# Kernel optimization log

Measured on AMD Instinct MI355X. Metric: run time of the kernel, lower is better.

The kernel has to match this reference:

```python
import jax, jax.numpy as jnp
import numpy as np
from jax import lax

L = 50      # observation_len
P = 30      # pred_len
N = 2048    # num nearby obstacles
EMB = 64    # embed_size
NH = 128    # node_hidden_size
EH = 256    # edge_hidden_size
AD = 64     # attention_dim
CNN = 2048  # resnet50 fc.in_features


def setup_inputs() -> dict:
    key = jax.random.key(0)
    ks = jax.random.split(key, 20)
    def rn(k, shape, s=1.0):
        return jax.random.normal(k, shape, jnp.float32) * s
    w = 0.05
    return {
        "img_embedding": rn(ks[0], (1, CNN)),
        "target_obs_pos": rn(ks[1], (1, L, 2)),
        "target_obs_pos_rel": rn(ks[2], (1, L, 2)),
        "nearby_obs_pos": rn(ks[3], (1, N, L, 2)),
        "nearby_obs_pos_rel": rn(ks[4], (1, N, L, 2)),
        "nearby_obs_hist_sizes": jax.random.randint(ks[5], (1, N, 1), 0, L + 1),
        "target_obs_hist_size": L,
        "target_h0": rn(ks[6], (NH,), w),
        "target_c0": rn(ks[7], (NH,), w),
        "W_temb": rn(ks[8], (2, EMB), w), "b_temb": jnp.zeros((EMB,), jnp.float32),
        "Wih_t": rn(ks[9], (EMB, 4 * NH), w), "Whh_t": rn(ks[10], (NH, 4 * NH), w),
        "bih_t": jnp.zeros((4 * NH,), jnp.float32), "bhh_t": jnp.zeros((4 * NH,), jnp.float32),
        "W_tatt": rn(ks[11], (2, AD), w), "b_tatt": jnp.zeros((AD,), jnp.float32),
        "nearby_h0": rn(ks[12], (EH,), w),
        "nearby_c0": rn(ks[13], (EH,), w),
        "W_nemb": rn(ks[14], (2, EMB), w), "b_nemb": jnp.zeros((EMB,), jnp.float32),
        "Wih_n": rn(ks[15], (EMB, 4 * EH), w), "Whh_n": rn(ks[16], (EH, 4 * EH), w),
        "bih_n": jnp.zeros((4 * EH,), jnp.float32), "bhh_n": jnp.zeros((4 * EH,), jnp.float32),
        "W_natt": rn(ks[17], (2, AD), w), "b_natt": jnp.zeros((AD,), jnp.float32),
        "W_pred": rn(ks[18], (NH + CNN + EH, 2), w), "b_pred": jnp.zeros((2,), jnp.float32),
    }


def _lstm_cell(x, h, c, Wih, Whh, bih, bhh, H):
    # PyTorch LSTM gate order: i, f, g, o
    g = x @ Wih + h @ Whh + bih + bhh
    i = jax.nn.sigmoid(g[..., :H])
    f = jax.nn.sigmoid(g[..., H:2 * H])
    gg = jnp.tanh(g[..., 2 * H:3 * H])
    o = jax.nn.sigmoid(g[..., 3 * H:])
    c2 = f * c + i * gg
    return o * jnp.tanh(c2), c2


def _forward(img_embedding, target_obs_pos, target_obs_pos_rel, nearby_obs_pos,
             nearby_obs_pos_rel, target_h0, target_c0, W_temb, b_temb,
             Wih_t, Whh_t, bih_t, bhh_t, W_tatt, b_tatt,
             nearby_h0, nearby_c0, W_nemb, b_nemb,
             Wih_n, Whh_n, bih_n, bhh_n, W_natt, b_natt,
             W_pred, b_pred, nearby_obs_hist_sizes, target_obs_hist_size):
    nhist = nearby_obs_hist_sizes.reshape(N)
    inv_sqrt_d = 1.0 / jnp.sqrt(jnp.float32(AD))

    def attention(trel, tpos, npos, nh, nmask, Ht_prev):
        # scores scaled by curr_N / sqrt(attention_dim), softmax over masked nearby.
        # max-subtracted softmax is mathematically identical to the original exp/sum.
        currN = jnp.sum(nmask.astype(jnp.float32))
        an = (tpos - npos) @ W_natt + b_natt          # [N, AD]
        at = trel @ W_tatt + b_tatt                   # [AD]
        scores = (an @ at) * currN * inv_sqrt_d       # [N]
        w = jax.nn.softmax(jnp.where(nmask, scores, -1e30))
        return jnp.where(currN >= 1.0, w @ nh, Ht_prev)

    def obs_step(carry, x):
        th, tc, nh, nc, Ht = carry
        t, tpos, trel, npos, nrel = x
        tmask = target_obs_hist_size > (L - t)
        nmask = nhist > (L - t)
        th2, tc2 = _lstm_cell(trel @ W_temb + b_temb, th, tc, Wih_t, Whh_t, bih_t, bhh_t, NH)
        th = jnp.where(tmask, th2, th)
        tc = jnp.where(tmask, tc2, tc)
        nh2, nc2 = _lstm_cell(nrel @ W_nemb + b_nemb, nh, nc, Wih_n, Whh_n, bih_n, bhh_n, EH)
        m = nmask[:, None]
        nh = jnp.where(m, nh2, nh)
        nc = jnp.where(m, nc2, nc)
        Ht = attention(trel, tpos, npos, nh, nmask, Ht)
        return (th, tc, nh, nc, Ht), None

    np_tm = jnp.swapaxes(nearby_obs_pos[0], 0, 1)      # [L, N, 2] time-major
    nr_tm = jnp.swapaxes(nearby_obs_pos_rel[0], 0, 1)
    xs = (jnp.arange(1, L), target_obs_pos[0, 1:], target_obs_pos_rel[0, 1:],
          np_tm[1:], nr_tm[1:])
    init = (target_h0, target_c0,
            jnp.broadcast_to(nearby_h0, (N, EH)),
            jnp.broadcast_to(nearby_c0, (N, EH)),
            nearby_h0)
    (th, tc, nh, nc, Ht), _ = lax.scan(obs_step, init, xs)

    # During prediction the original reuses nearby pos/rel from the last obs step.
    npos_last = nearby_obs_pos[0, :, L - 1, :]
    nrel_last = nearby_obs_pos_rel[0, :, L - 1, :]
    xn_last = nrel_last @ W_nemb + b_nemb
    all_mask = jnp.ones((N,), bool)

    def pred_step(carry, _):
        th, tc, nh, nc, Ht, pos = carry
        pred = jnp.concatenate([th, img_embedding[0], Ht]) @ W_pred + b_pred  # [2]
        pos = pos + pred
        th, tc = _lstm_cell(pred @ W_temb + b_temb, th, tc, Wih_t, Whh_t, bih_t, bhh_t, NH)
        nh, nc = _lstm_cell(xn_last, nh, nc, Wih_n, Whh_n, bih_n, bhh_n, EH)
        Ht = attention(pred, pos, npos_last, nh, all_mask, Ht)
        return (th, tc, nh, nc, Ht, pos), pred

    carry0 = (th, tc, nh, nc, Ht, target_obs_pos[0, L - 1])
    _, preds = lax.scan(pred_step, carry0, None, length=P)
    return preds[None]                                 # [1, P, 2]


def reference(img_embedding, target_obs_pos, target_obs_pos_rel, nearby_obs_pos,
              nearby_obs_pos_rel, nearby_obs_hist_sizes, target_obs_hist_size,
              target_h0, target_c0, W_temb, b_temb, Wih_t, Whh_t, bih_t, bhh_t,
              W_tatt, b_tatt, nearby_h0, nearby_c0, W_nemb, b_nemb,
              Wih_n, Whh_n, bih_n, bhh_n, W_natt, b_natt, W_pred, b_pred):
    return _forward(img_embedding, target_obs_pos, target_obs_pos_rel, nearby_obs_pos,
                    nearby_obs_pos_rel, target_h0, target_c0, W_temb, b_temb,
                    Wih_t, Whh_t, bih_t, bhh_t, W_tatt, b_tatt,
                    nearby_h0, nearby_c0, W_nemb, b_nemb,
                    Wih_n, Whh_n, bih_n, bhh_n, W_natt, b_natt,
                    W_pred, b_pred, nearby_obs_hist_sizes, target_obs_hist_size)
```

## Files before the change

kernel.cpp:

```cpp
#include <hip/hip_runtime.h>
#include <hip/hip_bf16.h>
#include <cstdint>

#define LH   50
#define PP   30
#define NAG  2048
#define NHID 128
#define EHID 256
#define ADIM 64
#define CNND 2048

typedef __attribute__((ext_vector_type(8))) short bf16x8;
typedef __attribute__((ext_vector_type(4))) float f32x4;

enum : int {
  WS_WT  = 0,
  WS_WZ  = 65536,
  WS_WHT = 131072,
  WS_WFN = 163840,
  WS_BFN = 165888,
  WS_WFT = 166912,
  WS_BFT = 167936,
  WS_TH  = 168448,
  WS_TC  = 168576,
  WS_W49 = 168704,
  WS_CN  = 170752,
  WS_Z   = 170756,
  WS_END = 293636
};

#define HLROW 280

__device__ __forceinline__ float sigf(float x){ return 1.0f/(1.0f + __expf(-x)); }
__device__ __forceinline__ float tanhfast(float x){
  x = fminf(15.0f, fmaxf(-15.0f, x));
  float e = __expf(2.0f*x);
  return (e - 1.0f)/(e + 1.0f);
}
__device__ __forceinline__ float bfs(short s){
  return __uint_as_float(((unsigned)(unsigned short)s) << 16);
}
__device__ __forceinline__ void gld16(const void* g, void* l){
  __builtin_amdgcn_global_load_lds(
      (const __attribute__((address_space(1))) unsigned int*)g,
      (__attribute__((address_space(3))) unsigned int*)l, 16, 0, 0);
}

__global__ void k_prep(const float* __restrict__ Whhn, const float* __restrict__ Whht,
                       const float* __restrict__ Wnemb, const float* __restrict__ bnemb,
                       const float* __restrict__ Wihn,  const float* __restrict__ bihn,
                       const float* __restrict__ bhhn,
                       const float* __restrict__ Wtemb, const float* __restrict__ btemb,
                       const float* __restrict__ Wiht,  const float* __restrict__ biht,
                       const float* __restrict__ bhht,
                       float* __restrict__ ws)
{
  const int b = blockIdx.x, tid = threadIdx.x;
  if (b < 128){
    __shared__ float t[32][33];
    __hip_bfloat16* WT = (__hip_bfloat16*)(ws + WS_WT);
    const int tx = tid & 31, ty = tid >> 5;
    const int j0 = (b & 31) << 5;
    const int e0 = (b >> 5) << 5;
    #pragma unroll
    for (int r = 0; r < 4; ++r)
      t[ty + 8*r][tx] = Whhn[(e0 + ty + 8*r)*1024 + j0 + tx];
    __syncthreads();
    const int c = e0 >> 5;
    #pragma unroll
    for (int r = 0; r < 4; ++r)
      WT[c*32768 + (j0 + ty + 8*r)*32 + tx] = __float2bfloat16(t[tx][ty + 8*r]);
  } else if (b < 192){
    __hip_bfloat16* WZ = (__hip_bfloat16*)(ws + WS_WZ);
    const int bb = b - 128;
    const int c  = bb >> 4;
    const int r0 = (bb & 15) << 5;
    const int r  = r0 + (tid >> 3);
    const int p  = tid & 7;
    const int ls = p ^ (r & 7);
    const int j  = ((ls >> 2) << 9) + r;
    const int kb = (4 + c)*32 + (ls & 3)*8;
    #pragma unroll
    for (int i = 0; i < 8; ++i)
      WZ[((c*512 + r)*8 + p)*8 + i] = __float2bfloat16(Whhn[(kb + i)*1024 + j]);
  } else {
    for (int j = tid; j < 1024; j += 256){
      float a0=0.f, a1=0.f, ab=0.f;
      for (int k=0;k<64;k++){
        const float w = Wihn[k*1024 + j];
        a0 += Wnemb[k]*w; a1 += Wnemb[64+k]*w; ab += bnemb[k]*w;
      }
      ws[WS_WFN + j]        = a0;
      ws[WS_WFN + 1024 + j] = a1;
      ws[WS_BFN + j]        = ab + bihn[j] + bhhn[j];
    }
    for (int j = tid; j < 512; j += 256){
      float a0=0.f, a1=0.f, ab=0.f;
      for (int k=0;k<64;k++){
        const float w = Wiht[k*512 + j];
        a0 += Wtemb[k]*w; a1 += Wtemb[64+k]*w; ab += btemb[k]*w;
      }
      ws[WS_WFT + j]       = a0;
      ws[WS_WFT + 512 + j] = a1;
      ws[WS_BFT + j]       = ab + biht[j] + bhht[j];
    }
    __hip_bfloat16* WTt = (__hip_bfloat16*)(ws + WS_WHT);
    for (int j = tid; j < 512; j += 256)
      for (int k = 0; k < 128; ++k)
        WTt[j*128 + k] = __float2bfloat16(Whht[k*512 + j]);
  }
}

__global__ __launch_bounds__(512, 2) void k_phaseA(
    const float* __restrict__ nh0, const float* __restrict__ nc0,
    const float* __restrict__ nrel, const int* __restrict__ nhist,
    const float* __restrict__ Wpred,
    const float* __restrict__ trel, const int* __restrict__ thsp,
    const float* __restrict__ Whht, const float* __restrict__ th0,
    const float* __restrict__ tc0,
    const float* __restrict__ tpos, const float* __restrict__ npos,
    const float* __restrict__ Wtatt, const float* __restrict__ btatt,
    const float* __restrict__ Wnatt, const float* __restrict__ bnatt,
    float* __restrict__ ws)
{
  extern __shared__ char smem_raw[];
  const int b = blockIdx.x, tid = threadIdx.x;
  const int wv = tid >> 6, lane = tid & 63;
  const int lhi = lane >> 4, llo = lane & 15;

  if (b < 128){
    short* wbuf = (short*)smem_raw;
    short* Hl   = (short*)(smem_raw + 131072);
    float* relS = (float*)(smem_raw + 131072 + 16*HLROW*2);
    float* vS   = relS + 1600;
    const int n0 = b << 4;

    {
      const char* wz = (const char*)(ws + WS_WZ);
      #pragma unroll
      for (int bufc = 0; bufc < 2; ++bufc){
        const char* gsrc = wz + bufc*65536 + wv*8192 + lane*16;
        char* ldst = smem_raw + bufc*65536 + wv*8192;
        #pragma unroll
        for (int i = 0; i < 8; ++i) gld16(gsrc + i*1024, ldst + i*1024);
      }
    }
    bf16x8 wreg[4][2][4];
    {
      const short* wt = (const short*)(ws + WS_WT);
      #pragma unroll
      for (int g = 0; g < 4; ++g)
        #pragma unroll
        for (int t = 0; t < 2; ++t){
          const int j = g*256 + (wv<<5) + t*16 + llo;
          #pragma unroll
          for (int ks = 0; ks < 4; ++ks)
            wreg[g][t][ks] = *(const bf16x8*)(wt + ks*32768 + j*32 + lhi*8);
        }
    }
    for (int i = tid; i < 1600; i += 512){
      const int a = i / 100, r = i % 100;
      relS[a*100 + r] = nrel[(n0 + a)*100 + r];
    }
    if (tid < 256){
      vS[2*tid]   = Wpred[2*(NHID + CNND + tid)];
      vS[2*tid+1] = Wpred[2*(NHID + CNND + tid) + 1];
    }
    for (int i = tid; i < 4096; i += 512){
      const int a = i >> 8, e = i & 255;
      ((__hip_bfloat16*)Hl)[a*HLROW + e] = __float2bfloat16(nh0[e]);
    }
    float wf0[4][2], wf1[4][2], wb[4][2];
    #pragma unroll
    for (int g = 0; g < 4; ++g)
      #pragma unroll
      for (int t = 0; t < 2; ++t){
        const int j = g*256 + (wv<<5) + t*16 + llo;
        wf0[g][t] = ws[WS_WFN + j];
        wf1[g][t] = ws[WS_WFN + 1024 + j];
        wb [g][t] = ws[WS_BFN + j];
      }
    float C[4][2], ho[4][2];
    #pragma unroll
    for (int r = 0; r < 4; ++r)
      #pragma unroll
      for (int t = 0; t < 2; ++t){
        const int eo = (wv<<5) + t*16 + llo;
        C[r][t]  = nc0[eo];
        ho[r][t] = nh0[eo];
      }
    int nh4[4];
    #pragma unroll
    for (int r = 0; r < 4; ++r) nh4[r] = nhist[n0 + lhi*4 + r];

    __syncthreads();

    for (int st = 1; st <= 78; ++st){
      const int thr  = (st <= 49) ? (50 - st) : -1;
      const int tsel = (st <= 49) ? st : 49;

      f32x4 acc[4][2];
      #pragma unroll
      for (int g = 0; g < 4; ++g)
        #pragma unroll
        for (int t = 0; t < 2; ++t) acc[g][t] = (f32x4){0.f,0.f,0.f,0.f};

      #pragma unroll
      for (int ks = 0; ks < 4; ++ks){
        const bf16x8 afr = *(const bf16x8*)(Hl + llo*HLROW + ks*32 + lhi*8);
        #pragma unroll
        for (int g = 0; g < 4; ++g)
          #pragma unroll
          for (int t = 0; t < 2; ++t)
            acc[g][t] = __builtin_amdgcn_mfma_f32_16x16x32_bf16(afr, wreg[g][t][ks], acc[g][t], 0,0,0);
      }

      #pragma unroll
      for (int i = 0; i < 4; ++i){
        const bf16x8 afs = *(const bf16x8*)(Hl + llo*HLROW + (4+i)*32 + lhi*8);
        asm volatile("s_waitcnt vmcnt(8)" ::: "memory");
        __builtin_amdgcn_sched_barrier(0);
        __builtin_amdgcn_s_barrier();
        __builtin_amdgcn_sched_barrier(0);
        const short* bb = wbuf + (i & 1)*32768;
        #pragma unroll
        for (int g = 0; g < 4; ++g)
          #pragma unroll
          for (int t = 0; t < 2; ++t){
            const int r  = ((g & 1) << 8) + (wv << 5) + t*16 + llo;
            const int ls = ((g >> 1) << 2) + lhi;
            const int p  = ls ^ (r & 7);
            const bf16x8 bfv = *(const bf16x8*)(bb + r*64 + p*8);
            acc[g][t] = __builtin_amdgcn_mfma_f32_16x16x32_bf16(afs, bfv, acc[g][t], 0,0,0);
          }
        asm volatile("s_waitcnt lgkmcnt(0)" ::: "memory");
        __builtin_amdgcn_sched_barrier(0);
        __builtin_amdgcn_s_barrier();
        __builtin_amdgcn_sched_barrier(0);
        {
          const int nc = (i + 2) & 3;
          const char* gsrc = (const char*)(ws + WS_WZ) + nc*65536 + wv*8192 + lane*16;
          char* ldst = smem_raw + (i & 1)*65536 + wv*8192;
          #pragma unroll
          for (int q = 0; q < 8; ++q) gld16(gsrc + q*1024, ldst + q*1024);
        }
      }

      #pragma unroll
      for (int r = 0; r < 4; ++r){
        const float r0 = relS[(lhi*4 + r)*100 + 2*tsel];
        const float r1 = relS[(lhi*4 + r)*100 + 2*tsel + 1];
        const bool mk = nh4[r] > thr;
        #pragma unroll
        for (int t = 0; t < 2; ++t){
          const float gi = acc[0][t][r] + r0*wf0[0][t] + r1*wf1[0][t] + wb[0][t];
          const float gf = acc[1][t][r] + r0*wf0[1][t] + r1*wf1[1][t] + wb[1][t];
          const float gg = acc[2][t][r] + r0*wf0[2][t] + r1*wf1[2][t] + wb[2][t];
          const float go = acc[3][t][r] + r0*wf0[3][t] + r1*wf1[3][t] + wb[3][t];
          const float c2 = sigf(gf)*C[r][t] + sigf(gi)*tanhfast(gg);
          const float h2 = sigf(go)*tanhfast(c2);
          if (mk){ C[r][t] = c2; ho[r][t] = h2; }
        }
      }
      #pragma unroll
      for (int r = 0; r < 4; ++r)
        #pragma unroll
        for (int t = 0; t < 2; ++t)
          ((__hip_bfloat16*)Hl)[(lhi*4 + r)*HLROW + (wv<<5) + t*16 + llo] =
              __float2bfloat16(ho[r][t]);
      asm volatile("s_waitcnt lgkmcnt(0)" ::: "memory");
      __builtin_amdgcn_sched_barrier(0);
      __builtin_amdgcn_s_barrier();
      __builtin_amdgcn_sched_barrier(0);

      if (st >= 49){
        const int s = st - 49;
        const int a = wv*2 + (lane >> 5);
        const int sub = lane & 31;
        float z0 = 0.f, z1 = 0.f;
        const short* hp = Hl + a*HLROW + sub*8;
        #pragma unroll
        for (int i = 0; i < 8; ++i){
          const float h = bfs(hp[i]);
          z0 += h*vS[2*(sub*8 + i)];
          z1 += h*vS[2*(sub*8 + i) + 1];
        }
        #pragma unroll
        for (int o = 16; o > 0; o >>= 1){
          z0 += __shfl_down(z0, o, 32);
          z1 += __shfl_down(z1, o, 32);
        }
        if (sub == 0){
          ws[WS_Z + (s*NAG + n0 + a)*2]     = z0;
          ws[WS_Z + (s*NAG + n0 + a)*2 + 1] = z1;
        }
      }
    }
  }
  else if (b == 128){
    float* hT = (float*)smem_raw;
    float* cT = hT + 128;
    float* gT = cT + 128;
    if (tid < 128){ hT[tid] = th0[tid]; cT[tid] = tc0[tid]; }
    __syncthreads();
    const int ths = thsp[0];
    for (int t = 1; t < 50; ++t){
      const float x0 = trel[2*t], x1 = trel[2*t+1];
      float acc = x0*ws[WS_WFT + tid] + x1*ws[WS_WFT + 512 + tid] + ws[WS_BFT + tid];
      for (int k = 0; k < 128; ++k) acc += hT[k]*Whht[k*512 + tid];
      gT[tid] = acc;
      __syncthreads();
      if (tid < 128 && ths > 50 - t){
        const float ig = sigf(gT[tid]),          fg = sigf(gT[128 + tid]);
        const float gg = tanhfast(gT[256 + tid]), og = sigf(gT[384 + tid]);
        const float c2 = fg*cT[tid] + ig*gg;
        cT[tid] = c2; hT[tid] = og*tanhfast(c2);
      }
      __syncthreads();
    }
    if (tid < 128){ ws[WS_TH + tid] = hT[tid]; ws[WS_TC + tid] = cT[tid]; }
  }
  else {
    float* at  = (float*)smem_raw;
    float* red = at + 64;
    float* uv  = red + 512;
    const int t = LH - 1;
    const float tr0 = trel[2*t], tr1 = trel[2*t+1];
    const float tp0 = tpos[2*t], tp1 = tpos[2*t+1];
    if (tid < ADIM) at[tid] = tr0*Wtatt[tid] + tr1*Wtatt[ADIM+tid] + btatt[tid];
    int cnt = 0;
    #pragma unroll
    for (int i = 0; i < 4; ++i) cnt += (nhist[tid + 512*i] > (LH - t)) ? 1 : 0;
    red[tid] = (float)cnt;
    __syncthreads();
    if (tid == 0){
      float u0=0.f,u1=0.f,v=0.f;
      for (int k=0;k<ADIM;k++){ u0 += Wnatt[k]*at[k]; u1 += Wnatt[ADIM+k]*at[k]; v += bnatt[k]*at[k]; }
      uv[0]=u0; uv[1]=u1; uv[2]=v;
    }
    for (int s = 256; s > 0; s >>= 1){ if (tid < s) red[tid] += red[tid+s]; __syncthreads(); }
    const float currN = red[0];
    __syncthreads();
    const float u0 = uv[0], u1 = uv[1], v = uv[2];
    const float scale = currN * 0.125f;
    float sc[4]; float smax = -3.0e38f;
    #pragma unroll
    for (int i = 0; i < 4; ++i){
      const int n = tid + 512*i;
      const float p0 = npos[n*100 + 2*t], p1 = npos[n*100 + 2*t + 1];
      float s = scale * ((tp0-p0)*u0 + (tp1-p1)*u1 + v);
      s = (nhist[n] > (LH - t)) ? s : -1.0e30f;
      sc[i] = s; smax = fmaxf(smax, s);
    }
    red[tid] = smax; __syncthreads();
    for (int s = 256; s > 0; s >>= 1){ if (tid<s) red[tid] = fmaxf(red[tid], red[tid+s]); __syncthreads(); }
    smax = red[0]; __syncthreads();
    float ssum = 0.f;
    #pragma unroll
    for (int i = 0; i < 4; ++i){ sc[i] = __expf(sc[i]-smax); ssum += sc[i]; }
    red[tid] = ssum; __syncthreads();
    for (int s = 256; s > 0; s >>= 1){ if (tid<s) red[tid] += red[tid+s]; __syncthreads(); }
    const float inv = 1.0f / red[0];
    #pragma unroll
    for (int i = 0; i < 4; ++i) ws[WS_W49 + tid + 512*i] = sc[i]*inv;
    if (tid == 0) ws[WS_CN] = currN;
  }
}

template<int K>
__device__ __forceinline__ void bredN(const float* v, volatile float* scratch,
                                      volatile float* outv, int tid){
  const int lane = tid & 63, wv = tid >> 6;
  #pragma unroll
  for (int k = 0; k < K; ++k){
    float x = v[k];
    #pragma unroll
    for (int o = 32; o > 0; o >>= 1) x += __shfl_down(x, o, 64);
    if (lane == 0) scratch[k*8 + wv] = x;
  }
  __syncthreads();
  if (tid == 0){
    #pragma unroll
    for (int k = 0; k < K; ++k){
      float s = 0.f;
      for (int i = 0; i < 8; ++i) s += scratch[k*8 + i];
      outv[k] = s;
    }
  }
  __syncthreads();
}

__device__ __forceinline__ float bredMax1(float x, volatile float* scratch,
                                          volatile float* outv, int tid){
  const int lane = tid & 63, wv = tid >> 6;
  #pragma unroll
  for (int o = 32; o > 0; o >>= 1) x = fmaxf(x, __shfl_down(x, o, 64));
  if (lane == 0) scratch[wv] = x;
  __syncthreads();
  if (tid == 0){
    float s = -3.0e38f;
    for (int i = 0; i < 8; ++i) s = fmaxf(s, scratch[i]);
    outv[0] = s;
  }
  __syncthreads();
  return outv[0];
}

__global__ __launch_bounds__(512, 1) void k_phaseB(
    const float* __restrict__ img, const float* __restrict__ tpos,
    const float* __restrict__ npos, const float* __restrict__ nh0,
    const float* __restrict__ Wpred, const float* __restrict__ bpred,
    const float* __restrict__ Wtatt, const float* __restrict__ btatt,
    const float* __restrict__ Wnatt, const float* __restrict__ bnatt,
    float* __restrict__ ws, float* __restrict__ out)
{
  __shared__ float p0s[NAG], p1s[NAG];
  __shared__ float th[128], tc[128], gl[512], at[64];
  __shared__ float scratch[24];
  __shared__ float bc[8];
  const int tid = threadIdx.x, lane = tid & 63, wv = tid >> 6;

  bf16x8 wreg[16];
  {
    const short* wp = (const short*)(ws + WS_WHT) + tid*128;
    #pragma unroll
    for (int f = 0; f < 16; ++f) wreg[f] = *(const bf16x8*)(wp + f*8);
  }
  for (int n = tid; n < NAG; n += 512){
    p0s[n] = npos[n*100 + 98];
    p1s[n] = npos[n*100 + 99];
  }
  if (tid < 128){ th[tid] = ws[WS_TH + tid]; tc[tid] = ws[WS_TC + tid]; }

  {
    float v[2] = {0.f, 0.f};
    for (int k = tid; k < CNND; k += 512){
      v[0] += img[k]*Wpred[2*(128 + k)];
      v[1] += img[k]*Wpred[2*(128 + k) + 1];
    }
    bredN<2>(v, scratch, bc, tid);
  }
  const float imgW0 = bc[0], imgW1 = bc[1];
  {
    float v[2] = {0.f, 0.f};
    if (tid < 256){
      v[0] = nh0[tid]*Wpred[2*(128 + CNND + tid)];
      v[1] = nh0[tid]*Wpred[2*(128 + CNND + tid) + 1];
    }
    bredN<2>(v, scratch, bc + 2, tid);
  }
  const float fb0 = bc[2], fb1 = bc[3];
  const float currN = ws[WS_CN];
  float pos0 = tpos[98], pos1 = tpos[99];
  float u0 = 0.f, u1 = 0.f, A = 0.f;
  __syncthreads();

  for (int s = 0; s < PP; ++s){
    const float* zs = ws + WS_Z + s*(NAG*2);
    float hv0, hv1;
    if (s == 0){
      if (currN >= 1.0f){
        float v[2] = {0.f, 0.f};
        for (int n = tid; n < NAG; n += 512){
          const float w = ws[WS_W49 + n];
          v[0] += w*zs[2*n]; v[1] += w*zs[2*n + 1];
        }
        bredN<2>(v, scratch, bc, tid);
        hv0 = bc[0]; hv1 = bc[1];
      } else { hv0 = fb0; hv1 = fb1; }
    } else {
      float sc[4], mx = -3.0e38f;
      #pragma unroll
      for (int i = 0; i < 4; ++i){
        const int n = tid + 512*i;
        sc[i] = 256.0f * (A - (p0s[n]*u0 + p1s[n]*u1));
        mx = fmaxf(mx, sc[i]);
      }
      mx = bredMax1(mx, scratch, bc + 7, tid);
      float v[3] = {0.f, 0.f, 0.f};
      #pragma unroll
      for (int i = 0; i < 4; ++i){
        const int n = tid + 512*i;
        const float e = __expf(sc[i] - mx);
        v[0] += e; v[1] += e*zs[2*n]; v[2] += e*zs[2*n + 1];
      }
      bredN<3>(v, scratch, bc, tid);
      const float inv = 1.0f / bc[0];
      hv0 = bc[1]*inv; hv1 = bc[2]*inv;
    }
    {
      float v[2] = {0.f, 0.f};
      if (tid < 128){
        v[0] = th[tid]*Wpred[2*tid];
        v[1] = th[tid]*Wpred[2*tid + 1];
      }
      bredN<2>(v, scratch, bc + 2, tid);
    }
    const float pr0 = bc[2] + imgW0 + hv0 + bpred[0];
    const float pr1 = bc[3] + imgW1 + hv1 + bpred[1];
    if (tid == 0){ out[2*s] = pr0; out[2*s + 1] = pr1; }
    pos0 += pr0; pos1 += pr1;

    {
      float g = pr0*ws[WS_WFT + tid] + pr1*ws[WS_WFT + 512 + tid] + ws[WS_BFT + tid];
      #pragma unroll
      for (int f = 0; f < 16; ++f){
        #pragma unroll
        for (int i = 0; i < 8; ++i)
          g += bfs(wreg[f][i]) * th[f*8 + i];
      }
      gl[tid] = g;
    }
    __syncthreads();
    float hnew = 0.f, cnew = 0.f;
    if (tid < 128){
      const float ig = sigf(gl[tid]),           fg = sigf(gl[128 + tid]);
      const float gg = tanhfast(gl[256 + tid]), og = sigf(gl[384 + tid]);
      cnew = fg*tc[tid] + ig*gg;
      hnew = og*tanhfast(cnew);
    }
    __syncthreads();
    if (tid < 128){ th[tid] = hnew; tc[tid] = cnew; }

    if (tid < ADIM) at[tid] = pr0*Wtatt[tid] + pr1*Wtatt[ADIM + tid] + btatt[tid];
    __syncthreads();
    if (wv == 0){
      float uu0 = Wnatt[lane]*at[lane];
      float uu1 = Wnatt[ADIM + lane]*at[lane];
      float vv  = bnatt[lane]*at[lane];
      #pragma unroll
      for (int o = 32; o > 0; o >>= 1){
        uu0 += __shfl_down(uu0, o, 64);
        uu1 += __shfl_down(uu1, o, 64);
        vv  += __shfl_down(vv,  o, 64);
      }
      if (lane == 0){
        bc[4] = uu0; bc[5] = uu1;
        bc[6] = pos0*uu0 + pos1*uu1 + vv;
      }
    }
    __syncthreads();
    u0 = bc[4]; u1 = bc[5]; A = bc[6];
  }
}

extern "C" void kernel_launch(void* const* d_in, const int* in_sizes, int n_in,
                              void* d_out, int out_size, void* d_ws, size_t ws_size,
                              hipStream_t stream) {
  const float* img   = (const float*)d_in[0];
  const float* tpos  = (const float*)d_in[1];
  const float* trel  = (const float*)d_in[2];
  const float* npos  = (const float*)d_in[3];
  const float* nrel  = (const float*)d_in[4];
  const int*   nhist = (const int*)d_in[5];
  const int*   ths   = (const int*)d_in[6];
  const float* th0   = (const float*)d_in[7];
  const float* tc0   = (const float*)d_in[8];
  const float* Wtemb = (const float*)d_in[9];
  const float* btemb = (const float*)d_in[10];
  const float* Wiht  = (const float*)d_in[11];
  const float* Whht  = (const float*)d_in[12];
  const float* biht  = (const float*)d_in[13];
  const float* bhht  = (const float*)d_in[14];
  const float* Wtatt = (const float*)d_in[15];
  const float* btatt = (const float*)d_in[16];
  const float* nh0   = (const float*)d_in[17];
  const float* nc0   = (const float*)d_in[18];
  const float* Wnemb = (const float*)d_in[19];
  const float* bnemb = (const float*)d_in[20];
  const float* Wihn  = (const float*)d_in[21];
  const float* Whhn  = (const float*)d_in[22];
  const float* bihn  = (const float*)d_in[23];
  const float* bhhn  = (const float*)d_in[24];
  const float* Wnatt = (const float*)d_in[25];
  const float* bnatt = (const float*)d_in[26];
  const float* Wpred = (const float*)d_in[27];
  const float* bpred = (const float*)d_in[28];
  float* ws  = (float*)d_ws;
  float* out = (float*)d_out;

  const int ldsA = 131072 + 16*HLROW*2 + 1600*4 + 512*4;

  k_prep<<<193, 256, 0, stream>>>(Whhn, Whht, Wnemb, bnemb, Wihn, bihn, bhhn,
                                  Wtemb, btemb, Wiht, biht, bhht, ws);
  k_phaseA<<<130, 512, ldsA, stream>>>(nh0, nc0, nrel, nhist, Wpred,
                                       trel, ths, Whht, th0, tc0,
                                       tpos, npos, Wtatt, btatt, Wnatt, bnatt, ws);
  k_phaseB<<<1, 512, 0, stream>>>(img, tpos, npos, nh0, Wpred, bpred,
                                  Wtatt, btatt, Wnatt, bnatt, ws, out);
}
```

Baseline: 937.6 us.

## Stream second half of nearby-LSTM recurrent weights from replicated global copies

```diff
diff --git a/kernel.cpp b/kernel.cpp
--- a/kernel.cpp
+++ b/kernel.cpp
@@ -15,21 +15,19 @@
 
 enum : int {
   WS_WT  = 0,
-  WS_WZ  = 65536,
-  WS_WHT = 131072,
-  WS_WFN = 163840,
-  WS_BFN = 165888,
-  WS_WFT = 166912,
-  WS_BFT = 167936,
-  WS_TH  = 168448,
-  WS_TC  = 168576,
-  WS_W49 = 168704,
-  WS_CN  = 170752,
-  WS_Z   = 170756,
-  WS_END = 293636
+  WS_WC  = 65536,
+  WS_WHT = 1114112,
+  WS_WFN = 1146880,
+  WS_BFN = 1148928,
+  WS_WFT = 1149952,
+  WS_BFT = 1150976,
+  WS_TH  = 1151488,
+  WS_TC  = 1151616,
+  WS_W49 = 1151744,
+  WS_CN  = 1153792,
+  WS_Z   = 1153796,
+  WS_END = 1276676
 };
-
-#define HLROW 280
 
 __device__ __forceinline__ float sigf(float x){ return 1.0f/(1.0f + __expf(-x)); }
 __device__ __forceinline__ float tanhfast(float x){
@@ -39,11 +37,6 @@
 }
 __device__ __forceinline__ float bfs(short s){
   return __uint_as_float(((unsigned)(unsigned short)s) << 16);
-}
-__device__ __forceinline__ void gld16(const void* g, void* l){
-  __builtin_amdgcn_global_load_lds(
-      (const __attribute__((address_space(1))) unsigned int*)g,
-      (__attribute__((address_space(3))) unsigned int*)l, 16, 0, 0);
 }
 
 __global__ void k_prep(const float* __restrict__ Whhn, const float* __restrict__ Whht,
@@ -56,9 +49,8 @@
                        float* __restrict__ ws)
 {
   const int b = blockIdx.x, tid = threadIdx.x;
-  if (b < 128){
+  if (b < 256){
     __shared__ float t[32][33];
-    __hip_bfloat16* WT = (__hip_bfloat16*)(ws + WS_WT);
     const int tx = tid & 31, ty = tid >> 5;
     const int j0 = (b & 31) << 5;
     const int e0 = (b >> 5) << 5;
@@ -67,22 +59,12 @@
       t[ty + 8*r][tx] = Whhn[(e0 + ty + 8*r)*1024 + j0 + tx];
     __syncthreads();
     const int c = e0 >> 5;
+    __hip_bfloat16* dst = (c < 4)
+        ? (__hip_bfloat16*)(ws + WS_WT) + c*32768
+        : (__hip_bfloat16*)(ws + WS_WC) + (c-4)*32768;
     #pragma unroll
     for (int r = 0; r < 4; ++r)
-      WT[c*32768 + (j0 + ty + 8*r)*32 + tx] = __float2bfloat16(t[tx][ty + 8*r]);
-  } else if (b < 192){
-    __hip_bfloat16* WZ = (__hip_bfloat16*)(ws + WS_WZ);
-    const int bb = b - 128;
-    const int c  = bb >> 4;
-    const int r0 = (bb & 15) << 5;
-    const int r  = r0 + (tid >> 3);
-    const int p  = tid & 7;
-    const int ls = p ^ (r & 7);
-    const int j  = ((ls >> 2) << 9) + r;
-    const int kb = (4 + c)*32 + (ls & 3)*8;
-    #pragma unroll
-    for (int i = 0; i < 8; ++i)
-      WZ[((c*512 + r)*8 + p)*8 + i] = __float2bfloat16(Whhn[(kb + i)*1024 + j]);
+      dst[(j0 + ty + 8*r)*32 + tx] = __float2bfloat16(t[tx][ty + 8*r]);
   } else {
     for (int j = tid; j < 1024; j += 256){
       float a0=0.f, a1=0.f, ab=0.f;
@@ -109,6 +91,14 @@
       for (int k = 0; k < 128; ++k)
         WTt[j*128 + k] = __float2bfloat16(Whht[k*512 + j]);
   }
+}
+
+__global__ void k_dup(float* __restrict__ ws)
+{
+  const int i = blockIdx.x*256 + threadIdx.x;
+  const int m  = 1 + (i >> 14);
+  const int si = (i & 16383)*4;
+  *(float4*)(ws + WS_WC + m*65536 + si) = *(const float4*)(ws + WS_WC + si);
 }
 
 __global__ __launch_bounds__(512, 2) void k_phaseA(
@@ -123,28 +113,21 @@
     const float* __restrict__ Wnatt, const float* __restrict__ bnatt,
     float* __restrict__ ws)
 {
-  extern __shared__ char smem_raw[];
+  __shared__ short Hl[16*264];
+  __shared__ float relS[1600];
+  __shared__ float vS[512];
+  __shared__ float wfS[3072];
   const int b = blockIdx.x, tid = threadIdx.x;
   const int wv = tid >> 6, lane = tid & 63;
   const int lhi = lane >> 4, llo = lane & 15;
 
   if (b < 128){
-    short* wbuf = (short*)smem_raw;
-    short* Hl   = (short*)(smem_raw + 131072);
-    float* relS = (float*)(smem_raw + 131072 + 16*HLROW*2);
-    float* vS   = relS + 1600;
-    const int n0 = b << 4;
-
-    {
-      const char* wz = (const char*)(ws + WS_WZ);
-      #pragma unroll
-      for (int bufc = 0; bufc < 2; ++bufc){
-        const char* gsrc = wz + bufc*65536 + wv*8192 + lane*16;
-        char* ldst = smem_raw + bufc*65536 + wv*8192;
-        #pragma unroll
-        for (int i = 0; i < 8; ++i) gld16(gsrc + i*1024, ldst + i*1024);
-      }
-    }
+    const int n0  = b << 4;
+    const int rot = (b >> 4) & 3;
+    const int cid = (b & 7)*2 + ((b >> 3) & 1);
+    const short* wst = (const short*)(ws + WS_WC) + cid*131072;
+    const int jcol = (wv << 5) + llo;
+
     bf16x8 wreg[4][2][4];
     {
       const short* wt = (const short*)(ws + WS_WT);
@@ -152,10 +135,22 @@
       for (int g = 0; g < 4; ++g)
         #pragma unroll
         for (int t = 0; t < 2; ++t){
-          const int j = g*256 + (wv<<5) + t*16 + llo;
+          const int j = g*256 + jcol + t*16;
           #pragma unroll
           for (int ks = 0; ks < 4; ++ks)
             wreg[g][t][ks] = *(const bf16x8*)(wt + ks*32768 + j*32 + lhi*8);
+        }
+    }
+    bf16x8 s0[8], s1[8];
+    {
+      const int cA = (rot) & 3, cB = (1 + rot) & 3;
+      #pragma unroll
+      for (int g = 0; g < 4; ++g)
+        #pragma unroll
+        for (int t = 0; t < 2; ++t){
+          const int j = g*256 + jcol + t*16;
+          s0[g*2+t] = *(const bf16x8*)(wst + cA*32768 + j*32 + lhi*8);
+          s1[g*2+t] = *(const bf16x8*)(wst + cB*32768 + j*32 + lhi*8);
         }
     }
     for (int i = tid; i < 1600; i += 512){
@@ -166,29 +161,21 @@
       vS[2*tid]   = Wpred[2*(NHID + CNND + tid)];
       vS[2*tid+1] = Wpred[2*(NHID + CNND + tid) + 1];
     }
+    for (int i = tid; i < 1024; i += 512){
+      wfS[i]        = ws[WS_WFN + i];
+      wfS[1024 + i] = ws[WS_WFN + 1024 + i];
+      wfS[2048 + i] = ws[WS_BFN + i];
+    }
     for (int i = tid; i < 4096; i += 512){
       const int a = i >> 8, e = i & 255;
-      ((__hip_bfloat16*)Hl)[a*HLROW + e] = __float2bfloat16(nh0[e]);
-    }
-    float wf0[4][2], wf1[4][2], wb[4][2];
-    #pragma unroll
-    for (int g = 0; g < 4; ++g)
-      #pragma unroll
-      for (int t = 0; t < 2; ++t){
-        const int j = g*256 + (wv<<5) + t*16 + llo;
-        wf0[g][t] = ws[WS_WFN + j];
-        wf1[g][t] = ws[WS_WFN + 1024 + j];
-        wb [g][t] = ws[WS_BFN + j];
-      }
-    float C[4][2], ho[4][2];
+      ((__hip_bfloat16*)Hl)[a*264 + e] = __float2bfloat16(nh0[e]);
+    }
+    float C[4][2];
     #pragma unroll
     for (int r = 0; r < 4; ++r)
       #pragma unroll
-      for (int t = 0; t < 2; ++t){
-        const int eo = (wv<<5) + t*16 + llo;
-        C[r][t]  = nc0[eo];
-        ho[r][t] = nh0[eo];
-      }
+      for (int t = 0; t < 2; ++t)
+        C[r][t] = nc0[jcol + t*16];
     int nh4[4];
     #pragma unroll
     for (int r = 0; r < 4; ++r) nh4[r] = nhist[n0 + lhi*4 + r];
@@ -207,67 +194,78 @@
 
       #pragma unroll
       for (int ks = 0; ks < 4; ++ks){
-        const bf16x8 afr = *(const bf16x8*)(Hl + llo*HLROW + ks*32 + lhi*8);
+        const bf16x8 afr = *(const bf16x8*)(Hl + llo*264 + ks*32 + lhi*8);
         #pragma unroll
         for (int g = 0; g < 4; ++g)
           #pragma unroll
           for (int t = 0; t < 2; ++t)
             acc[g][t] = __builtin_amdgcn_mfma_f32_16x16x32_bf16(afr, wreg[g][t][ks], acc[g][t], 0,0,0);
       }
-
       #pragma unroll
       for (int i = 0; i < 4; ++i){
-        const bf16x8 afs = *(const bf16x8*)(Hl + llo*HLROW + (4+i)*32 + lhi*8);
-        asm volatile("s_waitcnt vmcnt(8)" ::: "memory");
-        __builtin_amdgcn_sched_barrier(0);
-        __builtin_amdgcn_s_barrier();
-        __builtin_amdgcn_sched_barrier(0);
-        const short* bb = wbuf + (i & 1)*32768;
+        const int cs  = 4 + ((i + rot) & 3);
+        const int c2o = ((i + 2 + rot) & 3)*32768;
+        const bf16x8 afs = *(const bf16x8*)(Hl + llo*264 + cs*32 + lhi*8);
+        if ((i & 1) == 0){
+          #pragma unroll
+          for (int g = 0; g < 4; ++g)
+            #pragma unroll
+            for (int t = 0; t < 2; ++t)
+              acc[g][t] = __builtin_amdgcn_mfma_f32_16x16x32_bf16(afs, s0[g*2+t], acc[g][t], 0,0,0);
+          #pragma unroll
+          for (int g = 0; g < 4; ++g)
+            #pragma unroll
+            for (int t = 0; t < 2; ++t)
+              s0[g*2+t] = *(const bf16x8*)(wst + c2o + (g*256 + jcol + t*16)*32 + lhi*8);
+        } else {
+          #pragma unroll
+          for (int g = 0; g < 4; ++g)
+            #pragma unroll
+            for (int t = 0; t < 2; ++t)
+              acc[g][t] = __builtin_amdgcn_mfma_f32_16x16x32_bf16(afs, s1[g*2+t], acc[g][t], 0,0,0);
+          #pragma unroll
+          for (int g = 0; g < 4; ++g)
+            #pragma unroll
+            for (int t = 0; t < 2; ++t)
+              s1[g*2+t] = *(const bf16x8*)(wst + c2o + (g*256 + jcol + t*16)*32 + lhi*8);
+        }
+      }
+
+      asm volatile("s_waitcnt lgkmcnt(0)" ::: "memory");
+      __builtin_amdgcn_sched_barrier(0);
+      __builtin_amdgcn_s_barrier();
+      __builtin_amdgcn_sched_barrier(0);
+
+      {
+        float wfa[4][2], wfb[4][2], wbb[4][2];
         #pragma unroll
         for (int g = 0; g < 4; ++g)
           #pragma unroll
           for (int t = 0; t < 2; ++t){
-            const int r  = ((g & 1) << 8) + (wv << 5) + t*16 + llo;
-            const int ls = ((g >> 1) << 2) + lhi;
-            const int p  = ls ^ (r & 7);
-            const bf16x8 bfv = *(const bf16x8*)(bb + r*64 + p*8);
-            acc[g][t] = __builtin_amdgcn_mfma_f32_16x16x32_bf16(afs, bfv, acc[g][t], 0,0,0);
+            const int j = g*256 + jcol + t*16;
+            wfa[g][t] = wfS[j]; wfb[g][t] = wfS[1024 + j]; wbb[g][t] = wfS[2048 + j];
           }
-        asm volatile("s_waitcnt lgkmcnt(0)" ::: "memory");
-        __builtin_amdgcn_sched_barrier(0);
-        __builtin_amdgcn_s_barrier();
-        __builtin_amdgcn_sched_barrier(0);
-        {
-          const int nc = (i + 2) & 3;
-          const char* gsrc = (const char*)(ws + WS_WZ) + nc*65536 + wv*8192 + lane*16;
-          char* ldst = smem_raw + (i & 1)*65536 + wv*8192;
-          #pragma unroll
-          for (int q = 0; q < 8; ++q) gld16(gsrc + q*1024, ldst + q*1024);
-        }
-      }
-
-      #pragma unroll
-      for (int r = 0; r < 4; ++r){
-        const float r0 = relS[(lhi*4 + r)*100 + 2*tsel];
-        const float r1 = relS[(lhi*4 + r)*100 + 2*tsel + 1];
-        const bool mk = nh4[r] > thr;
-        #pragma unroll
-        for (int t = 0; t < 2; ++t){
-          const float gi = acc[0][t][r] + r0*wf0[0][t] + r1*wf1[0][t] + wb[0][t];
-          const float gf = acc[1][t][r] + r0*wf0[1][t] + r1*wf1[1][t] + wb[1][t];
-          const float gg = acc[2][t][r] + r0*wf0[2][t] + r1*wf1[2][t] + wb[2][t];
-          const float go = acc[3][t][r] + r0*wf0[3][t] + r1*wf1[3][t] + wb[3][t];
-          const float c2 = sigf(gf)*C[r][t] + sigf(gi)*tanhfast(gg);
-          const float h2 = sigf(go)*tanhfast(c2);
-          if (mk){ C[r][t] = c2; ho[r][t] = h2; }
-        }
-      }
-      #pragma unroll
-      for (int r = 0; r < 4; ++r)
-        #pragma unroll
-        for (int t = 0; t < 2; ++t)
-          ((__hip_bfloat16*)Hl)[(lhi*4 + r)*HLROW + (wv<<5) + t*16 + llo] =
-              __float2bfloat16(ho[r][t]);
+        #pragma unroll
+        for (int r = 0; r < 4; ++r){
+          const int ag = lhi*4 + r;
+          const float r0 = relS[ag*100 + 2*tsel];
+          const float r1 = relS[ag*100 + 2*tsel + 1];
+          const bool mk = nh4[r] > thr;
+          #pragma unroll
+          for (int t = 0; t < 2; ++t){
+            const float gi = acc[0][t][r] + r0*wfa[0][t] + r1*wfb[0][t] + wbb[0][t];
+            const float gf = acc[1][t][r] + r0*wfa[1][t] + r1*wfb[1][t] + wbb[1][t];
+            const float gg = acc[2][t][r] + r0*wfa[2][t] + r1*wfb[2][t] + wbb[2][t];
+            const float go = acc[3][t][r] + r0*wfa[3][t] + r1*wfb[3][t] + wbb[3][t];
+            const float c2 = sigf(gf)*C[r][t] + sigf(gi)*tanhfast(gg);
+            const float h2 = sigf(go)*tanhfast(c2);
+            if (mk){
+              C[r][t] = c2;
+              ((__hip_bfloat16*)Hl)[ag*264 + jcol + t*16] = __float2bfloat16(h2);
+            }
+          }
+        }
+      }
       asm volatile("s_waitcnt lgkmcnt(0)" ::: "memory");
       __builtin_amdgcn_sched_barrier(0);
       __builtin_amdgcn_s_barrier();
@@ -278,7 +276,7 @@
         const int a = wv*2 + (lane >> 5);
         const int sub = lane & 31;
         float z0 = 0.f, z1 = 0.f;
-        const short* hp = Hl + a*HLROW + sub*8;
+        const short* hp = Hl + a*264 + sub*8;
         #pragma unroll
         for (int i = 0; i < 8; ++i){
           const float h = bfs(hp[i]);
@@ -298,9 +296,9 @@
     }
   }
   else if (b == 128){
-    float* hT = (float*)smem_raw;
-    float* cT = hT + 128;
-    float* gT = cT + 128;
+    float* hT = relS;
+    float* cT = relS + 128;
+    float* gT = relS + 256;
     if (tid < 128){ hT[tid] = th0[tid]; cT[tid] = tc0[tid]; }
     __syncthreads();
     const int ths = thsp[0];
@@ -321,9 +319,9 @@
     if (tid < 128){ ws[WS_TH + tid] = hT[tid]; ws[WS_TC + tid] = cT[tid]; }
   }
   else {
-    float* at  = (float*)smem_raw;
-    float* red = at + 64;
-    float* uv  = red + 512;
+    float* at  = vS;
+    float* red = relS;
+    float* uv  = vS + 64;
     const int t = LH - 1;
     const float tr0 = trel[2*t], tr1 = trel[2*t+1];
     const float tp0 = tpos[2*t], tp1 = tpos[2*t+1];
@@ -579,13 +577,12 @@
   float* ws  = (float*)d_ws;
   float* out = (float*)d_out;
 
-  const int ldsA = 131072 + 16*HLROW*2 + 1600*4 + 512*4;
-
-  k_prep<<<193, 256, 0, stream>>>(Whhn, Whht, Wnemb, bnemb, Wihn, bihn, bhhn,
+  k_prep<<<257, 256, 0, stream>>>(Whhn, Whht, Wnemb, bnemb, Wihn, bihn, bhhn,
                                   Wtemb, btemb, Wiht, biht, bhht, ws);
-  k_phaseA<<<130, 512, ldsA, stream>>>(nh0, nc0, nrel, nhist, Wpred,
-                                       trel, ths, Whht, th0, tc0,
-                                       tpos, npos, Wtatt, btatt, Wnatt, bnatt, ws);
+  k_dup<<<960, 256, 0, stream>>>(ws);
+  k_phaseA<<<130, 512, 0, stream>>>(nh0, nc0, nrel, nhist, Wpred,
+                                    trel, ths, Whht, th0, tc0,
+                                    tpos, npos, Wtatt, btatt, Wnatt, bnatt, ws);
   k_phaseB<<<1, 512, 0, stream>>>(img, tpos, npos, nh0, Wpred, bpred,
                                   Wtatt, btatt, Wnatt, bnatt, ws, out);
 }
```

Result: slower. 1.117 ms (+19.1%).
